# Performance work log

Hardware: AMD Instinct MI355X
Metric: run time of the kernel (lower is better)

The kernel has to match this reference:

```python
import math
import jax, jax.numpy as jnp
import numpy as np

N_HEADS = 16   # matches init_kwargs n_heads
C_SAMPLING = 1  # matches init_kwargs c_sampling


def setup_inputs() -> dict:
    rng = jax.random.key(0)
    ks = jax.random.split(rng, 8)
    L = S = 2048
    B = 8
    D = 1024
    sc = 0.02  # weight scale
    return {
        "query": jax.random.normal(ks[0], (L, B, D), jnp.float32),
        "key": jax.random.normal(ks[1], (S, B, D), jnp.float32),
        "value": jax.random.normal(ks[2], (S, B, D), jnp.float32),
        "Wq": jax.random.normal(ks[3], (D, D), jnp.float32) * sc,
        "bq": jnp.zeros((D,), jnp.float32),
        "Wk": jax.random.normal(ks[4], (D, D), jnp.float32) * sc,
        "bk": jnp.zeros((D,), jnp.float32),
        "Wv": jax.random.normal(ks[5], (D, D), jnp.float32) * sc,
        "bv": jnp.zeros((D,), jnp.float32),
        "Wo": jax.random.normal(ks[6], (D, D), jnp.float32) * sc,
        "bo": jnp.zeros((D,), jnp.float32),
    }


def _autocorr_forward(query, key, value, Wq, bq, Wk, bk, Wv, bv, Wo, bo):
    L, B, D = query.shape
    S = key.shape[0]
    H = N_HEADS
    E = D // H

    def proj(x, W, b):
        return x @ W.T + b

    def to_attn(x):  # (T,B,D) -> (B,H,E,T)
        T = x.shape[0]
        return x.reshape(T, B, H, E).transpose(1, 2, 3, 0)

    Q = to_attn(proj(query, Wq, bq))   # (B,H,E,L)
    K = to_attn(proj(key, Wk, bk))     # (B,H,E,S)
    V = to_attn(proj(value, Wv, bv))   # (B,H,E,S)

    # Align K/V length to L (static shapes: branch resolved at trace time)
    if L > S:
        pad = [(0, 0)] * 3 + [(0, L - S)]
        K = jnp.pad(K, pad)
        V = jnp.pad(V, pad)
    else:
        K = K[..., :L]
        V = V[..., :L]

    # Cross-correlation via FFT along time axis
    Qf = jnp.fft.rfft(Q, axis=-1)
    Kf = jnp.fft.rfft(K, axis=-1)
    corr = jnp.fft.irfft(Qf * jnp.conj(Kf), n=L, axis=-1)  # (B,H,E,L)

    # --- time_delay_agg ---
    topk = int(C_SAMPLING * math.log(L))
    mean_corr = corr.mean(axis=-2)                         # (B,H,L)
    scores, taus = jax.lax.top_k(mean_corr, topk)          # (B,H,topk)
    w = jax.nn.softmax(scores, axis=-1)                    # (B,H,topk)
    # delayed index (s + tau) mod L : (B,H,L,topk)
    idx = (jnp.arange(L)[None, None, :, None] + taus[:, :, None, :]) % L
    # gather V along time: (B,H,E,L,topk)
    delayed = jnp.take_along_axis(V[:, :, :, :, None], idx[:, :, None, :, :], axis=3)
    agg = jnp.mean(delayed * w[:, :, None, None, :], axis=-1)  # (B,H,E,L)

    # recover_from_attn: (B,H,E,L) -> (L,B,H*E)
    out = agg.transpose(3, 0, 1, 2).reshape(L, B, H * E)
    return out @ Wo.T + bo  # (L,B,D); need_weights=False so corr is dropped


def reference(query, key, value, Wq, bq, Wk, bk, Wv, bv, Wo, bo):
    return _autocorr_forward(query, key, value, Wq, bq, Wk, bk, Wv, bv, Wo, bo)
```

## Files before the change

### kernel.cpp

```cpp
#include <hip/hip_runtime.h>
#include <math.h>

#define TOPK 7

typedef __attribute__((ext_vector_type(8))) short bf16x8;
typedef __attribute__((ext_vector_type(4))) float f32x4;

__device__ __forceinline__ void glds16(const ushort* g, ushort* l)
{
    __builtin_amdgcn_global_load_lds(
        (const __attribute__((address_space(1))) void*)g,
        (__attribute__((address_space(3))) void*)l, 16, 0, 0);
}

__device__ __forceinline__ void split1(float x, ushort& h, ushort& lo)
{
    union U { float f; unsigned u; };
    U a; a.f = x;
    unsigned r = (a.u + 0x7FFFu + ((a.u >> 16) & 1u)) >> 16;
    h = (ushort)r;
    U b; b.u = r << 16;
    U d; d.f = x - b.f;
    unsigned r2 = (d.u + 0x7FFFu + ((d.u >> 16) & 1u)) >> 16;
    lo = (ushort)r2;
}

__global__ __launch_bounds__(256)
void split_f32(const float* __restrict__ x, ushort* __restrict__ hi,
               ushort* __restrict__ lo, int n4)
{
    for (int i = blockIdx.x * 256 + threadIdx.x; i < n4; i += gridDim.x * 256) {
        float4 v = ((const float4*)x)[i];
        ushort4 h, lw;
        split1(v.x, h.x, lw.x);
        split1(v.y, h.y, lw.y);
        split1(v.z, h.z, lw.z);
        split1(v.w, h.w, lw.w);
        ((ushort4*)hi)[i] = h;
        ((ushort4*)lo)[i] = lw;
    }
}

__global__ __launch_bounds__(512, 2)
void gemm_split(const ushort* __restrict__ Ah, const ushort* __restrict__ Al,
                const ushort* __restrict__ Bh, const ushort* __restrict__ Bl,
                const float* __restrict__ bias, float* __restrict__ C)
{
    __shared__ ushort lds[65536];
    const int tid = threadIdx.x;
    const int w = tid >> 6, l = tid & 63;

    const int ord = blockIdx.y * gridDim.x + blockIdx.x;
    const int cpx = (gridDim.x * gridDim.y) >> 3;
    const int swzb = (ord & 7) * cpx + (ord >> 3);
    const int bx = swzb & 3;
    const int by = swzb >> 2;

    const int wm = w >> 2, wn = w & 3;
    const int lr = l & 15, kgr = l >> 4;

    const ushort* gbB[4]; size_t goB[4]; int loB[4];
    const ushort* gbA[4]; size_t goA[4]; int loA[4];
#pragma unroll
    for (int q = 0; q < 4; ++q) {
        int idx = w * 4 + q;
        int cb = idx >> 4;
        int kg = (idx >> 2) & 3;
        int rblk = idx & 3;
        gbB[q] = cb ? Bl : Bh;
        goB[q] = (size_t)(bx * 256 + rblk * 64 + l) * 1024 + kg * 8;
        loB[q] = 16384 + cb * 8192 + kg * 2048 + rblk * 512;
        gbA[q] = cb ? Al : Ah;
        goA[q] = (size_t)(by * 256 + rblk * 64 + l) * 1024 + kg * 8;
        loA[q] = cb * 8192 + kg * 2048 + rblk * 512;
    }

    f32x4 acc[8][4];
#pragma unroll
    for (int i = 0; i < 8; ++i)
#pragma unroll
        for (int j = 0; j < 4; ++j) acc[i][j] = (f32x4){0.f, 0.f, 0.f, 0.f};

#define STAGE_B(bufbase_, k0_) do { \
    const int _bb = (bufbase_); const int _kk = (k0_); \
    _Pragma("unroll") \
    for (int q = 0; q < 4; ++q) \
        glds16(gbB[q] + goB[q] + _kk, &lds[_bb + loB[q]]); \
} while (0)

#define STAGE_A2(bufbase_, k0_, qa_, qb_) do { \
    const int _bb = (bufbase_); const int _kk = (k0_); \
    glds16(gbA[qa_] + goA[qa_] + _kk, &lds[_bb + loA[qa_]]); \
    glds16(gbA[qb_] + goA[qb_] + _kk, &lds[_bb + loA[qb_]]); \
} while (0)

#define COMPUTE2(i0_) do { \
    _Pragma("unroll") \
    for (int ii = 0; ii < 2; ++ii) { \
        const int i = (i0_) + ii; \
        const int ra = wm * 128 + i * 16 + lr; \
        bf16x8 fah = *(const bf16x8*)&lb[       kgr * 2048 + ra * 8]; \
        bf16x8 fal = *(const bf16x8*)&lb[8192 + kgr * 2048 + ra * 8]; \
        __builtin_amdgcn_s_setprio(1); \
        _Pragma("unroll") \
        for (int j = 0; j < 4; ++j) \
            acc[i][j] = __builtin_amdgcn_mfma_f32_16x16x32_bf16(fah, fbh[j], acc[i][j], 0, 0, 0); \
        _Pragma("unroll") \
        for (int j = 0; j < 4; ++j) \
            acc[i][j] = __builtin_amdgcn_mfma_f32_16x16x32_bf16(fah, fbl[j], acc[i][j], 0, 0, 0); \
        _Pragma("unroll") \
        for (int j = 0; j < 4; ++j) \
            acc[i][j] = __builtin_amdgcn_mfma_f32_16x16x32_bf16(fal, fbh[j], acc[i][j], 0, 0, 0); \
        __builtin_amdgcn_s_setprio(0); \
    } \
} while (0)

    STAGE_B(0, 0);       STAGE_A2(0, 0, 0, 1);       STAGE_A2(0, 0, 2, 3);
    STAGE_B(32768, 32);  STAGE_A2(32768, 32, 0, 1);  STAGE_A2(32768, 32, 2, 3);
    asm volatile("s_waitcnt vmcnt(8)" ::: "memory");
    __builtin_amdgcn_s_barrier();

#pragma unroll 2
    for (int t = 0; t < 32; ++t) {
        const int cb = (t & 1) * 32768;
        const ushort* lb = &lds[cb];
        const bool pre = (t < 30);
        const int kn = (t + 2) * 32;

        bf16x8 fbh[4], fbl[4];
#pragma unroll
        for (int j = 0; j < 4; ++j) {
            int rb = wn * 64 + j * 16 + lr;
            fbh[j] = *(const bf16x8*)&lb[16384 + kgr * 2048 + rb * 8];
            fbl[j] = *(const bf16x8*)&lb[24576 + kgr * 2048 + rb * 8];
        }
        COMPUTE2(0);
        __builtin_amdgcn_s_barrier();

        if (pre) STAGE_B(cb, kn);
        COMPUTE2(2);
        __builtin_amdgcn_s_barrier();

        if (pre) STAGE_A2(cb, kn, 0, 2);
        COMPUTE2(4);
        __builtin_amdgcn_s_barrier();

        COMPUTE2(6);
        __builtin_amdgcn_s_barrier();
        if (pre) {
            STAGE_A2(cb, kn, 1, 3);
            asm volatile("s_waitcnt vmcnt(8)" ::: "memory");
        } else {
            asm volatile("s_waitcnt vmcnt(0)" ::: "memory");
        }
        __builtin_amdgcn_s_barrier();
    }
#undef STAGE_B
#undef STAGE_A2
#undef COMPUTE2

#pragma unroll
    for (int j = 0; j < 4; ++j) {
        int col = bx * 256 + wn * 64 + j * 16 + lr;
        float bb = bias[col];
#pragma unroll
        for (int i = 0; i < 8; ++i) {
            int row0 = by * 256 + wm * 128 + i * 16 + kgr * 4;
#pragma unroll
            for (int reg = 0; reg < 4; ++reg)
                C[(size_t)(row0 + reg) * 1024 + col] = acc[i][j][reg] + bb;
        }
    }
}

__global__ __launch_bounds__(256)
void transpose_bhet(const float* __restrict__ src, float* __restrict__ dst)
{
    __shared__ float tile[64][129];
    const int tid = threadIdx.x;
    const int bh = blockIdx.x;
    const int b = bh >> 4, h = bh & 15;
    const int t0 = blockIdx.y * 128;
    const float* sp = src + (size_t)(t0 * 8 + b) * 1024 + h * 64;
#pragma unroll
    for (int i = 0; i < 8; ++i) {
        int idx = i * 256 + tid;
        int t = idx >> 4;
        int e4 = (idx & 15) * 4;
        float4 v = *(const float4*)(sp + (size_t)t * 8192 + e4);
        tile[e4 + 0][t] = v.x; tile[e4 + 1][t] = v.y; tile[e4 + 2][t] = v.z; tile[e4 + 3][t] = v.w;
    }
    __syncthreads();
    float* dp = dst + (size_t)bh * 64 * 2048 + t0;
#pragma unroll
    for (int i = 0; i < 8; ++i) {
        int idx = i * 256 + tid;
        int e = idx >> 5;
        int t4 = (idx & 31) * 4;
        float4 o;
        o.x = tile[e][t4]; o.y = tile[e][t4 + 1]; o.z = tile[e][t4 + 2]; o.w = tile[e][t4 + 3];
        *(float4*)(dp + (size_t)e * 2048 + t4) = o;
    }
}

__device__ __forceinline__ float2 cadd(float2 a, float2 b){ return make_float2(a.x+b.x, a.y+b.y); }
__device__ __forceinline__ float2 csub(float2 a, float2 b){ return make_float2(a.x-b.x, a.y-b.y); }
__device__ __forceinline__ float2 cmul(float2 a, float2 b){ return make_float2(a.x*b.x - a.y*b.y, a.x*b.y + a.y*b.x); }

__device__ __forceinline__ int swz(int i) { return i ^ ((i >> 4) & 15); }

__device__ float2* fft2048(float2* x, float2* y, const float2* tw, int tid)
{
#pragma unroll 1
    for (int st = 0; st < 5; ++st) {
        const int s = 1 << (2 * st);
#pragma unroll
        for (int ui = 0; ui < 2; ++ui) {
            const int u = ui * 256 + tid;
            const int q = u & (s - 1);
            const int ps = u - q;
            float2 a = x[swz(u)],        b = x[swz(u + 512)];
            float2 c = x[swz(u + 1024)], d = x[swz(u + 1536)];
            float2 t0 = cadd(a, c), t1 = csub(a, c);
            float2 t2 = cadd(b, d), tb = csub(b, d);
            float2 t3 = make_float2(tb.y, -tb.x);
            float2 w1 = tw[ps];
            float2 w2 = tw[2 * ps];
            float2 w3 = cmul(w1, w2);
            const int o = 4 * ps + q;
            y[swz(o)]         = cadd(t0, t2);
            y[swz(o + s)]     = cmul(cadd(t1, t3), w1);
            y[swz(o + 2 * s)] = cmul(csub(t0, t2), w2);
            y[swz(o + 3 * s)] = cmul(csub(t1, t3), w3);
        }
        __syncthreads();
        float2* tsw = x; x = y; y = tsw;
    }
#pragma unroll
    for (int ui = 0; ui < 4; ++ui) {
        const int u = ui * 256 + tid;
        float2 a = x[swz(u)], b = x[swz(u + 1024)];
        y[swz(u)]        = cadd(a, b);
        y[swz(u + 1024)] = csub(a, b);
    }
    __syncthreads();
    return y;
}

__global__ __launch_bounds__(256)
void corr_fwd(const float* __restrict__ Qa, const float* __restrict__ Ka,
              float2* __restrict__ Spart)
{
    __shared__ float2 za[2048];
    __shared__ float2 zb[2048];
    __shared__ float2 tw[1024];
    const int tid = threadIdx.x;
    const int bh = blockIdx.x;
    const int eg = blockIdx.y;

#pragma unroll
    for (int r = 0; r < 4; ++r) {
        int u = tid + 256 * r;
        float sn, cs;
        sincospif((float)u * (1.0f / 1024.0f), &sn, &cs);
        tw[u] = make_float2(cs, -sn);
    }

    float2 sacc[4];
#pragma unroll
    for (int r = 0; r < 4; ++r) sacc[r] = make_float2(0.f, 0.f);
    float2 sacc1024 = make_float2(0.f, 0.f);

    const float* q0 = Qa + ((size_t)bh * 64 + eg * 8) * 2048;
    const float* k0 = Ka + ((size_t)bh * 64 + eg * 8) * 2048;

    for (int e = 0; e < 8; ++e) {
        const float* qr = q0 + (size_t)e * 2048;
        const float* kr = k0 + (size_t)e * 2048;
        for (int t = tid; t < 2048; t += 256)
            za[swz(t)] = make_float2(qr[t], kr[t]);
        __syncthreads();

        float2* res = fft2048(za, zb, tw, tid);

#pragma unroll
        for (int r = 0; r < 4; ++r) {
            int f = tid + 256 * r;
            float2 A  = res[swz(f)];
            float2 Bc = res[swz((2048 - f) & 2047)];
            float Ur = A.x + Bc.x, Ui = A.y - Bc.y;
            float Vr = A.x - Bc.x, Vi = -A.y - Bc.y;
            sacc[r].x += 0.25f * (-(Ur * Vi + Ui * Vr));
            sacc[r].y += 0.25f * ( Ur * Vr - Ui * Vi );
        }
        if (tid == 0) {
            float2 A = res[swz(1024)];
            float Ur = 2.f * A.x;
            float Vi = -2.f * A.y;
            sacc1024.x += 0.25f * (-(Ur * Vi));
            sacc1024.y += 0.25f * 0.f;
        }
        __syncthreads();
    }
    float2* sp = Spart + ((size_t)bh * 8 + eg) * 1025;
#pragma unroll
    for (int r = 0; r < 4; ++r) sp[tid + 256 * r] = sacc[r];
    if (tid == 0) sp[1024] = sacc1024;
}

__global__ __launch_bounds__(256)
void corr_inv_topk(const float2* __restrict__ Spart,
                   int* __restrict__ taus, float* __restrict__ wout)
{
    __shared__ float2 za[2048];
    __shared__ float2 zb[2048];
    __shared__ float2 tw[1024];
    __shared__ float2 Sh[1025];
    __shared__ float  redv[256];
    __shared__ int    redi[256];
    __shared__ float  sc[TOPK];
    __shared__ int    si[TOPK];

    const int tid = threadIdx.x;
    const int bh = blockIdx.x;

#pragma unroll
    for (int r = 0; r < 4; ++r) {
        int u = tid + 256 * r;
        float sn, cs;
        sincospif((float)u * (1.0f / 1024.0f), &sn, &cs);
        tw[u] = make_float2(cs, -sn);
    }

    const float2* sp0 = Spart + (size_t)bh * 8 * 1025;
    for (int f = tid; f < 1025; f += 256) {
        float2 s = make_float2(0.f, 0.f);
#pragma unroll
        for (int g = 0; g < 8; ++g) {
            float2 v = sp0[(size_t)g * 1025 + f];
            s.x += v.x; s.y += v.y;
        }
        Sh[f] = s;
    }
    __syncthreads();
    for (int f = tid; f < 2048; f += 256) {
        float2 v = (f <= 1024) ? make_float2(Sh[f].x, -Sh[f].y) : Sh[2048 - f];
        za[swz(f)] = v;
    }
    __syncthreads();

    float2* res = fft2048(za, zb, tw, tid);

    for (int k = 0; k < TOPK; ++k) {
        float bvv = -INFINITY; int bii = 0;
        for (int t = tid; t < 2048; t += 256) {
            float v = res[swz(t)].x;
            if (v > bvv) { bvv = v; bii = t; }
        }
        redv[tid] = bvv; redi[tid] = bii;
        __syncthreads();
        for (int off = 128; off > 0; off >>= 1) {
            if (tid < off) {
                float ov = redv[tid + off]; int oi = redi[tid + off];
                if (ov > redv[tid] || (ov == redv[tid] && oi < redi[tid])) { redv[tid] = ov; redi[tid] = oi; }
            }
            __syncthreads();
        }
        if (tid == 0) { sc[k] = redv[0]; si[k] = redi[0]; res[swz(redi[0])].x = -INFINITY; }
        __syncthreads();
    }
    if (tid == 0) {
        const float scale = 1.0f / (2048.0f * 64.0f);
        float m = sc[0] * scale;
        float ex[TOPK]; float ssum = 0.f;
        for (int k = 0; k < TOPK; ++k) { ex[k] = expf(sc[k] * scale - m); ssum += ex[k]; }
        for (int k = 0; k < TOPK; ++k) {
            taus[bh * TOPK + k] = si[k];
            wout[bh * TOPK + k] = ex[k] / ssum;
        }
    }
}

__global__ __launch_bounds__(256)
void agg_gather(const float* __restrict__ Vp, const int* __restrict__ taus,
                const float* __restrict__ w, ushort* __restrict__ ah,
                ushort* __restrict__ al)
{
    const int tid = threadIdx.x;
    const int bh = blockIdx.x;
    const int b = bh >> 4, h = bh & 15;
    const int t0 = blockIdx.y * 256;
    __shared__ int   stau[TOPK];
    __shared__ float sw[TOPK];
    if (tid < TOPK) { stau[tid] = taus[bh * TOPK + tid]; sw[tid] = w[bh * TOPK + tid] * (1.0f / TOPK); }
    __syncthreads();
    const float* vb = Vp + (size_t)b * 1024 + h * 64;
    ushort* ahb = ah + (size_t)b * 1024 + h * 64;
    ushort* alb = al + (size_t)b * 1024 + h * 64;
#pragma unroll
    for (int i = 0; i < 16; ++i) {
        int idx = i * 256 + tid;
        int t  = t0 + (idx >> 4);
        int e4 = (idx & 15) * 4;
        float a0 = 0.f, a1 = 0.f, a2 = 0.f, a3 = 0.f;
#pragma unroll
        for (int k = 0; k < TOPK; ++k) {
            int ts = (t + stau[k]) & 2047;
            float4 v = *(const float4*)(vb + (size_t)ts * 8192 + e4);
            a0 = fmaf(sw[k], v.x, a0); a1 = fmaf(sw[k], v.y, a1);
            a2 = fmaf(sw[k], v.z, a2); a3 = fmaf(sw[k], v.w, a3);
        }
        ushort4 hh, ll;
        split1(a0, hh.x, ll.x); split1(a1, hh.y, ll.y);
        split1(a2, hh.z, ll.z); split1(a3, hh.w, ll.w);
        *(ushort4*)(ahb + (size_t)t * 8192 + e4) = hh;
        *(ushort4*)(alb + (size_t)t * 8192 + e4) = ll;
    }
}

extern "C" void kernel_launch(void* const* d_in, const int* in_sizes, int n_in,
                              void* d_out, int out_size, void* d_ws, size_t ws_size,
                              hipStream_t stream)
{
    (void)in_sizes; (void)n_in; (void)out_size;
    const float* query = (const float*)d_in[0];
    const float* key   = (const float*)d_in[1];
    const float* value = (const float*)d_in[2];
    const float* Wq = (const float*)d_in[3];
    const float* bq = (const float*)d_in[4];
    const float* Wk = (const float*)d_in[5];
    const float* bk = (const float*)d_in[6];
    const float* Wv = (const float*)d_in[7];
    const float* bv = (const float*)d_in[8];
    const float* Wo = (const float*)d_in[9];
    const float* bo = (const float*)d_in[10];
    float* out = (float*)d_out;

    const size_t NEL  = (size_t)16777216;
    const size_t HEL  = NEL / 2;
    const size_t WEL  = (size_t)1048576;
    const size_t SLOTB = (size_t)64 * 1024 * 1024;

    char* ws = (char*)d_ws;
    float*  s1 = (float*)ws;
    char*   s2 = ws + SLOTB;
    char*   s3 = ws + 2 * SLOTB;
    int*    dtaus = (int*)(ws + 3 * SLOTB);
    float*  dw    = (float*)(dtaus + 128 * TOPK);
    const bool big_ws = ws_size >= 3 * SLOTB + (size_t)16 * 1024 * 1024;

    dim3 blk(256);
    dim3 gblk(512);
    dim3 gemm_full(4, 64), gemm_half(4, 32);
    dim3 tr_grid(128, 16);

    split_f32<<<1024, blk, 0, stream>>>(Wq, (ushort*)s3, (ushort*)s3 + WEL, (int)(WEL / 4));
    split_f32<<<2048, blk, 0, stream>>>(query, (ushort*)s2, (ushort*)s2 + NEL, (int)(NEL / 4));
    gemm_split<<<gemm_full, gblk, 0, stream>>>((ushort*)s2, (ushort*)s2 + NEL,
                                               (ushort*)s3, (ushort*)s3 + WEL, bq, s1);
    transpose_bhet<<<tr_grid, blk, 0, stream>>>(s1, (float*)s2);
    ushort* wkh = (ushort*)d_out;
    split_f32<<<1024, blk, 0, stream>>>(Wk, wkh, wkh + WEL, (int)(WEL / 4));
    split_f32<<<2048, blk, 0, stream>>>(key, (ushort*)s3, (ushort*)s3 + NEL, (int)(NEL / 4));
    gemm_split<<<gemm_full, gblk, 0, stream>>>((ushort*)s3, (ushort*)s3 + NEL,
                                               wkh, wkh + WEL, bk, s1);
    transpose_bhet<<<tr_grid, blk, 0, stream>>>(s1, (float*)s3);

    if (big_ws) {
        ushort* wvh = (ushort*)(ws + 3 * SLOTB + (size_t)8 * 1024 * 1024);
        split_f32<<<1024, blk, 0, stream>>>(Wv, wvh, wvh + WEL, (int)(WEL / 4));
        ushort* vsp = (ushort*)d_out;
        split_f32<<<2048, blk, 0, stream>>>(value, vsp, vsp + NEL, (int)(NEL / 4));
        gemm_split<<<gemm_full, gblk, 0, stream>>>(vsp, vsp + NEL, wvh, wvh + WEL,
                                                   bv, s1);
    } else {
        ushort* wvh = (ushort*)((char*)d_out + (size_t)32 * 1024 * 1024);
        split_f32<<<1024, blk, 0, stream>>>(Wv, wvh, wvh + WEL, (int)(WEL / 4));
        ushort* vsp = (ushort*)d_out;
        for (int hhalf = 0; hhalf < 2; ++hhalf) {
            split_f32<<<2048, blk, 0, stream>>>(value + hhalf * HEL, vsp, vsp + HEL, (int)(HEL / 4));
            gemm_split<<<gemm_half, gblk, 0, stream>>>(vsp, vsp + HEL, wvh, wvh + WEL,
                                                       bv, s1 + hhalf * HEL);
        }
    }

    float2* Spart = (float2*)d_out;
    corr_fwd<<<dim3(128, 8), blk, 0, stream>>>((const float*)s2, (const float*)s3, Spart);
    corr_inv_topk<<<dim3(128), blk, 0, stream>>>(Spart, dtaus, dw);
    agg_gather<<<dim3(128, 8), blk, 0, stream>>>(s1, dtaus, dw,
                                                 (ushort*)s2, (ushort*)s2 + NEL);
    split_f32<<<1024, blk, 0, stream>>>(Wo, (ushort*)s3, (ushort*)s3 + WEL, (int)(WEL / 4));
    gemm_split<<<gemm_full, gblk, 0, stream>>>((ushort*)s2, (ushort*)s2 + NEL,
                                               (ushort*)s3, (ushort*)s3 + WEL, bo, out);
}
```

Before: 626.1 us.

## Restructure GEMM main loop into load-then-MFMA phases with earlier A-tile prefetch

Splits each k-step of the split-bf16 GEMM into four phases. Each phase loads the A fragments from LDS, issues the global-to-LDS prefetch, waits on lgkmcnt behind a sched_barrier, then runs a block of MFMAs at raised priority. The last A quarter for the next buffer is now staged one iteration earlier, into the other buffer, so more global loads are in flight, and the vmcnt thresholds are adjusted to match. The aim is to overlap LDS reads and global prefetch with MFMA work better, at the cost of more fragment registers and a more fragile ordering of waits and barriers.

```diff
diff --git a/kernel.cpp b/kernel.cpp
--- a/kernel.cpp
+++ b/kernel.cpp
@@ -64,15 +64,15 @@
 #pragma unroll
     for (int q = 0; q < 4; ++q) {
         int idx = w * 4 + q;
-        int cb = idx >> 4;
+        int cbq = idx >> 4;
         int kg = (idx >> 2) & 3;
         int rblk = idx & 3;
-        gbB[q] = cb ? Bl : Bh;
+        gbB[q] = cbq ? Bl : Bh;
         goB[q] = (size_t)(bx * 256 + rblk * 64 + l) * 1024 + kg * 8;
-        loB[q] = 16384 + cb * 8192 + kg * 2048 + rblk * 512;
-        gbA[q] = cb ? Al : Ah;
+        loB[q] = 16384 + cbq * 8192 + kg * 2048 + rblk * 512;
+        gbA[q] = cbq ? Al : Ah;
         goA[q] = (size_t)(by * 256 + rblk * 64 + l) * 1024 + kg * 8;
-        loA[q] = cb * 8192 + kg * 2048 + rblk * 512;
+        loA[q] = cbq * 8192 + kg * 2048 + rblk * 512;
     }
 
     f32x4 acc[8][4];
@@ -94,62 +94,83 @@
     glds16(gbA[qb_] + goA[qb_] + _kk, &lds[_bb + loA[qb_]]); \
 } while (0)
 
-#define COMPUTE2(i0_) do { \
+#define LOADA(h_, l_, i_) do { \
+    const int _ra = wm * 128 + (i_) * 16 + lr; \
+    h_ = *(const bf16x8*)&lb[       kgr * 2048 + _ra * 8]; \
+    l_ = *(const bf16x8*)&lb[8192 + kgr * 2048 + _ra * 8]; \
+} while (0)
+
+#define MFMA3(i_, ah_, al_) do { \
     _Pragma("unroll") \
-    for (int ii = 0; ii < 2; ++ii) { \
-        const int i = (i0_) + ii; \
-        const int ra = wm * 128 + i * 16 + lr; \
-        bf16x8 fah = *(const bf16x8*)&lb[       kgr * 2048 + ra * 8]; \
-        bf16x8 fal = *(const bf16x8*)&lb[8192 + kgr * 2048 + ra * 8]; \
-        __builtin_amdgcn_s_setprio(1); \
-        _Pragma("unroll") \
-        for (int j = 0; j < 4; ++j) \
-            acc[i][j] = __builtin_amdgcn_mfma_f32_16x16x32_bf16(fah, fbh[j], acc[i][j], 0, 0, 0); \
-        _Pragma("unroll") \
-        for (int j = 0; j < 4; ++j) \
-            acc[i][j] = __builtin_amdgcn_mfma_f32_16x16x32_bf16(fah, fbl[j], acc[i][j], 0, 0, 0); \
-        _Pragma("unroll") \
-        for (int j = 0; j < 4; ++j) \
-            acc[i][j] = __builtin_amdgcn_mfma_f32_16x16x32_bf16(fal, fbh[j], acc[i][j], 0, 0, 0); \
-        __builtin_amdgcn_s_setprio(0); \
-    } \
+    for (int j = 0; j < 4; ++j) \
+        acc[i_][j] = __builtin_amdgcn_mfma_f32_16x16x32_bf16(ah_, fbh[j], acc[i_][j], 0, 0, 0); \
+    _Pragma("unroll") \
+    for (int j = 0; j < 4; ++j) \
+        acc[i_][j] = __builtin_amdgcn_mfma_f32_16x16x32_bf16(ah_, fbl[j], acc[i_][j], 0, 0, 0); \
+    _Pragma("unroll") \
+    for (int j = 0; j < 4; ++j) \
+        acc[i_][j] = __builtin_amdgcn_mfma_f32_16x16x32_bf16(al_, fbh[j], acc[i_][j], 0, 0, 0); \
 } while (0)
 
-    STAGE_B(0, 0);       STAGE_A2(0, 0, 0, 1);       STAGE_A2(0, 0, 2, 3);
-    STAGE_B(32768, 32);  STAGE_A2(32768, 32, 0, 1);  STAGE_A2(32768, 32, 2, 3);
-    asm volatile("s_waitcnt vmcnt(8)" ::: "memory");
+#define PHASE_SYNC() do { \
+    __builtin_amdgcn_s_barrier(); \
+    asm volatile("s_waitcnt lgkmcnt(0)" ::: "memory"); \
+    __builtin_amdgcn_sched_barrier(0); \
+} while (0)
+
+    STAGE_B(0, 0);      STAGE_A2(0, 0, 0, 2);      STAGE_A2(0, 0, 1, 3);
+    STAGE_B(32768, 32); STAGE_A2(32768, 32, 0, 2);
+    asm volatile("s_waitcnt vmcnt(6)" ::: "memory");
     __builtin_amdgcn_s_barrier();
 
 #pragma unroll 2
     for (int t = 0; t < 32; ++t) {
         const int cb = (t & 1) * 32768;
+        const int ob = cb ^ 32768;
         const ushort* lb = &lds[cb];
-        const bool pre = (t < 30);
-        const int kn = (t + 2) * 32;
+        const int kn1 = (t + 1) * 32;
+        const int kn2 = (t + 2) * 32;
 
         bf16x8 fbh[4], fbl[4];
+        bf16x8 ah0, al0, ah1, al1;
+
 #pragma unroll
         for (int j = 0; j < 4; ++j) {
             int rb = wn * 64 + j * 16 + lr;
             fbh[j] = *(const bf16x8*)&lb[16384 + kgr * 2048 + rb * 8];
             fbl[j] = *(const bf16x8*)&lb[24576 + kgr * 2048 + rb * 8];
         }
-        COMPUTE2(0);
+        LOADA(ah0, al0, 0); LOADA(ah1, al1, 1);
+        if (t < 31) STAGE_A2(ob, kn1, 1, 3);
+        PHASE_SYNC();
+        __builtin_amdgcn_s_setprio(1);
+        MFMA3(0, ah0, al0); MFMA3(1, ah1, al1);
+        __builtin_amdgcn_s_setprio(0);
         __builtin_amdgcn_s_barrier();
 
-        if (pre) STAGE_B(cb, kn);
-        COMPUTE2(2);
+        LOADA(ah0, al0, 2); LOADA(ah1, al1, 3);
+        if (t < 30) STAGE_B(cb, kn2);
+        PHASE_SYNC();
+        __builtin_amdgcn_s_setprio(1);
+        MFMA3(2, ah0, al0); MFMA3(3, ah1, al1);
+        __builtin_amdgcn_s_setprio(0);
         __builtin_amdgcn_s_barrier();
 
-        if (pre) STAGE_A2(cb, kn, 0, 2);
-        COMPUTE2(4);
+        LOADA(ah0, al0, 4); LOADA(ah1, al1, 5);
+        if (t < 30) STAGE_A2(cb, kn2, 0, 2);
+        PHASE_SYNC();
+        __builtin_amdgcn_s_setprio(1);
+        MFMA3(4, ah0, al0); MFMA3(5, ah1, al1);
+        __builtin_amdgcn_s_setprio(0);
         __builtin_amdgcn_s_barrier();
 
-        COMPUTE2(6);
-        __builtin_amdgcn_s_barrier();
-        if (pre) {
-            STAGE_A2(cb, kn, 1, 3);
-            asm volatile("s_waitcnt vmcnt(8)" ::: "memory");
+        LOADA(ah0, al0, 6); LOADA(ah1, al1, 7);
+        PHASE_SYNC();
+        __builtin_amdgcn_s_setprio(1);
+        MFMA3(6, ah0, al0); MFMA3(7, ah1, al1);
+        __builtin_amdgcn_s_setprio(0);
+        if (t < 30) {
+            asm volatile("s_waitcnt vmcnt(6)" ::: "memory");
         } else {
             asm volatile("s_waitcnt vmcnt(0)" ::: "memory");
         }
@@ -157,7 +178,9 @@
     }
 #undef STAGE_B
 #undef STAGE_A2
-#undef COMPUTE2
+#undef LOADA
+#undef MFMA3
+#undef PHASE_SYNC
 
 #pragma unroll
     for (int j = 0; j < 4; ++j) {
```

Result: no change. 635.7 us (+1.5%).
